# Optimization experiments

Hardware: AMD Instinct MI355X
Metric: run time of the kernel (lower is better)

Reference implementation:

```python
import jax, jax.numpy as jnp
import numpy as np

EPS = 1e-5       # BatchNorm2d eps
NHEAD = 8
FILL = -1e30     # stands in for scores_fill_value=-inf (finite for grad safety)


def _proj(x, w, b, g, beta, mean, var):
    # Conv2d 1x1 over NCHW (H=1) == channel matmul, followed by eval-mode BatchNorm2d.
    y = jnp.einsum('oc,bcht->boht', w, x) + b[None, :, None, None]
    inv = g * jax.lax.rsqrt(var + EPS)
    return y * inv[None, :, None, None] + (beta - mean * inv)[None, :, None, None]


def setup_inputs() -> dict:
    rng = jax.random.key(0)
    ks = jax.random.split(rng, 10)
    B, C, T = 8, 512, 1024
    query = jax.random.normal(ks[0], (B, C, 1, T), jnp.float32)
    key = jax.random.normal(ks[1], (B, C, 1, T), jnp.float32)
    value = jax.random.normal(ks[2], (B, C, 1, T), jnp.float32)
    mask = jax.random.randint(ks[3], (B, 1, T, T), 0, 2).astype(jnp.int32)
    Ws = jax.random.normal(ks[4], (4, C, C), jnp.float32) * (1.0 / np.sqrt(C))
    bs = jax.random.normal(ks[5], (4, C), jnp.float32) * 0.1
    gammas = jax.random.uniform(ks[6], (4, C), jnp.float32, 0.5, 1.5)
    betas = jax.random.normal(ks[7], (4, C), jnp.float32) * 0.1
    means = jax.random.normal(ks[8], (4, C), jnp.float32) * 0.1
    vars_ = jax.random.uniform(ks[9], (4, C), jnp.float32, 0.5, 1.5)
    return dict(query=query, key=key, value=value, mask=mask, Ws=Ws, bs=bs,
                gammas=gammas, betas=betas, means=means, vars_=vars_)


def reference(query, key, value, mask, Ws, bs, gammas, betas, means, vars_):
    B, C, _, T1 = query.shape
    T2 = key.shape[3]
    h = NHEAD
    d_k = C // h
    denom = 1.0 / np.sqrt(d_k)

    q = _proj(query, Ws[0], bs[0], gammas[0], betas[0], means[0], vars_[0]).reshape(B, h, d_k, T1)
    k = _proj(key,   Ws[1], bs[1], gammas[1], betas[1], means[1], vars_[1]).reshape(B, h, d_k, T2)
    v = _proj(value, Ws[2], bs[2], gammas[2], betas[2], means[2], vars_[2]).reshape(B, h, d_k, T2)

    # scores = k^T @ q -> (B, h, T2, T1); softmax over key axis (dim=2, matching torch)
    scores = jnp.einsum('bhds,bhdt->bhst', k, q) * denom
    mask0 = jnp.transpose(mask, (0, 1, 3, 2)) == 0  # (B, 1, T2, T1)
    scores = jnp.where(mask0, FILL, scores)
    attn = jax.nn.softmax(scores, axis=2)
    attn = jnp.where(mask0, 0.0, attn)

    # x = v @ attn -> (B, h, d_k, T1) -> (B, C, 1, T1)
    x = jnp.einsum('bhds,bhst->bhdt', v, attn).reshape(B, C, 1, T1)
    out = _proj(x, Ws[3], bs[3], gammas[3], betas[3], means[3], vars_[3])

    # cache=None branch: new_cache = cat(raw key, raw value) along channel dim
    new_cache = jnp.concatenate([key, value], axis=1)
    return (out, new_cache)
```

## Files before the change

kernel.cpp:

```cpp
#include <hip/hip_runtime.h>

typedef unsigned short u16;
typedef unsigned int   u32;
typedef short  bfrag   __attribute__((ext_vector_type(8)));
typedef float  accfrag __attribute__((ext_vector_type(16)));
typedef unsigned int   u32x4 __attribute__((ext_vector_type(4)));
typedef unsigned short u16x4 __attribute__((ext_vector_type(4)));
typedef float          f32x4 __attribute__((ext_vector_type(4)));

#define B_SZ 8
#define C_SZ 512
#define T_SZ 1024
#define NH   8
#define DK   64

#define QSCL 0.18033688f

__device__ __forceinline__ u16 f2bf(float f) {
  u32 u = __float_as_uint(f);
  u = u + 0x7fffu + ((u >> 16) & 1u);
  return (u16)(u >> 16);
}

__device__ __forceinline__ float fexp2(float x) {
  return __builtin_amdgcn_exp2f(x);
}

__device__ __forceinline__ u32 cvtpk(float lo, float hi) {
  u32 r;
  asm("v_cvt_pk_bf16_f32 %0, %1, %2" : "=v"(r) : "v"(lo), "v"(hi));
  return r;
}

__device__ __forceinline__ void permswap(u32 &a, u32 &b) {
  asm volatile("v_permlane32_swap_b32 %0, %1" : "+v"(a), "+v"(b));
}

__device__ __forceinline__ void gload16(const u16* g, u16* l) {
  __builtin_amdgcn_global_load_lds(
      (const __attribute__((address_space(1))) void*)g,
      (__attribute__((address_space(3))) void*)l, 16, 0, 0);
}

__global__ void prep_wb(const float* __restrict__ Ws, const float* __restrict__ bs,
                        const float* __restrict__ gam, const float* __restrict__ beta,
                        const float* __restrict__ mean, const float* __restrict__ var,
                        u16* __restrict__ Wp, float* __restrict__ bp) {
  int bx = blockIdx.x;
  if (bx < 4096) {
    int idx = bx * 256 + threadIdx.x;
    int io = idx >> 9;
    float inv = gam[io] * rsqrtf(var[io] + 1e-5f);
    Wp[idx] = f2bf(Ws[idx] * inv);
  } else {
    int idx = (bx - 4096) * 256 + threadIdx.x;
    float inv = gam[idx] * rsqrtf(var[idx] + 1e-5f);
    bp[idx] = bs[idx] * inv + beta[idx] - mean[idx] * inv;
  }
}

__global__ void transpose_cvt(const float* __restrict__ q, const float* __restrict__ k,
                              const float* __restrict__ v, u16* __restrict__ Xt,
                              float* __restrict__ cache) {
  __shared__ float tile[32][33];
  int z = blockIdx.z;
  int src = z >> 3, b = z & 7;
  const float* in = (src == 0) ? q : ((src == 1) ? k : v);
  u16* out = Xt + (size_t)src * ((size_t)B_SZ * T_SZ * C_SZ);
  int t0 = blockIdx.x * 32, c0 = blockIdx.y * 32;
  int cy  = threadIdx.x >> 3;
  int tx4 = threadIdx.x & 7;

  f32x4 v4 = *(const f32x4*)(in + (((size_t)b * C_SZ + c0 + cy) << 10) + t0 + tx4 * 4);
  if (src >= 1) {
    int cc = c0 + cy + (src == 2 ? 512 : 0);
    *(f32x4*)(cache + ((size_t)b << 20) + ((size_t)cc << 10) + t0 + tx4 * 4) = v4;
  }
  tile[cy][tx4 * 4 + 0] = v4[0];
  tile[cy][tx4 * 4 + 1] = v4[1];
  tile[cy][tx4 * 4 + 2] = v4[2];
  tile[cy][tx4 * 4 + 3] = v4[3];
  __syncthreads();
  float w0 = tile[tx4 * 4 + 0][cy];
  float w1 = tile[tx4 * 4 + 1][cy];
  float w2 = tile[tx4 * 4 + 2][cy];
  float w3 = tile[tx4 * 4 + 3][cy];
  u32 lo = cvtpk(w0, w1), hi = cvtpk(w2, w3);
  u32* orow = (u32*)(out + (((size_t)(b << 10) + t0 + cy) * C_SZ) + c0 + tx4 * 4);
  orow[0] = lo;
  orow[1] = hi;
}

__global__ void mask_bits(const int* __restrict__ mask, u32* __restrict__ mbT) {
  int gw   = (blockIdx.x * 256 + threadIdx.x) >> 6;
  int lane = threadIdx.x & 63;
  int bt   = gw >> 1;
  int half = gw & 1;
  const int* base = mask + ((size_t)bt << 10) + half * 512 + lane;
  int b = bt >> 10, t = bt & 1023;
  u32* obase = mbT + (((size_t)b * 32 + half * 16) << 10) + t;
#pragma unroll
  for (int j = 0; j < 8; ++j) {
    unsigned long long bal = __ballot(base[j * 64] != 0);
    if (lane == 0)  obase[(size_t)(2 * j + 0) << 10] = (u32)bal;
    if (lane == 32) obase[(size_t)(2 * j + 1) << 10] = (u32)(bal >> 32);
  }
}

__launch_bounds__(256, 4)
__global__ void gemm_qkv(const u16* __restrict__ Wp, const float* __restrict__ bpA,
                         const u16* __restrict__ Xt,
                         u16* __restrict__ Qf, u16* __restrict__ Kf, u16* __restrict__ Vf) {
  __shared__ __align__(16) u16 lds[2 * 128 * 64];
  int tid = threadIdx.x;
  int src = blockIdx.z >> 3;
  int b   = blockIdx.z & 7;
  int t0 = blockIdx.x * 128;
  int o0 = blockIdx.y * 128;
  int wid = tid >> 6, lane = tid & 63;
  int ln = lane & 31, hi = lane >> 5;
  int wr = wid >> 1, wc = wid & 1;

  const u16* Wsrc = Wp + (size_t)src * 262144;
  const float* bp = bpA + src * 512;
  const u16* Xin  = Xt + (size_t)src * ((size_t)B_SZ * T_SZ * C_SZ);
  u16* Yout = (src == 0) ? Qf : (src == 1 ? Kf : Vf);

  const char* Ag = (const char*)Wsrc;
  const char* Bg = (const char*)(Xin + (((size_t)b << 10) + t0) * C_SZ);
  char* ldsA = (char*)lds;
  char* ldsB = (char*)lds + 16384;

  accfrag acc[2][2];
#pragma unroll
  for (int m2 = 0; m2 < 2; ++m2)
#pragma unroll
    for (int n2 = 0; n2 < 2; ++n2)
#pragma unroll
      for (int e = 0; e < 16; ++e) acc[m2][n2][e] = 0.f;

  int lin = tid * 16;
  u32x4 ra[4], rb[4];
#pragma unroll
  for (int it = 0; it < 4; ++it) {
    int off = lin + it * 4096;
    int r = off >> 7, cb = off & 127;
    ra[it] = *(const u32x4*)(Ag + (size_t)(o0 + r) * 1024 + cb);
    rb[it] = *(const u32x4*)(Bg + (size_t)r * 1024 + cb);
  }

  for (int kt = 0; kt < 8; ++kt) {
    __syncthreads();
#pragma unroll
    for (int it = 0; it < 4; ++it) {
      int off = lin + it * 4096;
      int swz = off ^ (((off >> 7) & 7) << 4);
      *(u32x4*)(ldsA + swz) = ra[it];
      *(u32x4*)(ldsB + swz) = rb[it];
    }
    __syncthreads();
    if (kt < 7) {
#pragma unroll
      for (int it = 0; it < 4; ++it) {
        int off = lin + it * 4096;
        int r = off >> 7, cb = off & 127;
        ra[it] = *(const u32x4*)(Ag + (size_t)(o0 + r) * 1024 + (kt + 1) * 128 + cb);
        rb[it] = *(const u32x4*)(Bg + (size_t)r * 1024 + (kt + 1) * 128 + cb);
      }
    }
#pragma unroll
    for (int kk = 0; kk < 4; ++kk) {
      int csw = (kk * 32 + hi * 16) ^ ((ln & 7) << 4);
      bfrag a[2], bb[2];
#pragma unroll
      for (int m2 = 0; m2 < 2; ++m2)
        a[m2] = *(const bfrag*)(ldsA + (wr * 64 + m2 * 32 + ln) * 128 + csw);
#pragma unroll
      for (int n2 = 0; n2 < 2; ++n2)
        bb[n2] = *(const bfrag*)(ldsB + (wc * 64 + n2 * 32 + ln) * 128 + csw);
#pragma unroll
      for (int m2 = 0; m2 < 2; ++m2)
#pragma unroll
        for (int n2 = 0; n2 < 2; ++n2)
          acc[m2][n2] = __builtin_amdgcn_mfma_f32_32x32x16_bf16(a[m2], bb[n2], acc[m2][n2], 0, 0, 0);
    }
  }

  float oscl = (src == 0) ? QSCL : 1.0f;
#pragma unroll
  for (int m2 = 0; m2 < 2; ++m2) {
    int obase = o0 + wr * 64 + m2 * 32;
#pragma unroll
    for (int n2 = 0; n2 < 2; ++n2) {
      int t = t0 + wc * 64 + n2 * 32 + ln;
      if (src < 2) {
        int tt5 = t & 31, st = t >> 5;
#pragma unroll
        for (int g = 0; g < 4; ++g) {
          int d0 = obase + 8 * g + 4 * hi;
          int hh = d0 >> 6, dd = d0 & 63;
          u16x4 pk4;
#pragma unroll
          for (int qq = 0; qq < 4; ++qq)
            pk4[qq] = f2bf((acc[m2][n2][4 * g + qq] + bp[d0 + qq]) * oscl);
          size_t a = ((((size_t)b * 8 + hh) * 32 + st) << 11)
                   + (size_t)((dd >> 4) * 512 + (tt5 + 32 * ((dd >> 3) & 1)) * 8 + (dd & 7));
          *(u16x4*)(Yout + a) = pk4;
        }
      } else {
        int s = t, st = s >> 5;
#pragma unroll
        for (int r = 0; r < 16; ++r) {
          int d = obase + (r & 3) + 8 * (r >> 2) + 4 * hi;
          int hh = d >> 6, dd = d & 63;
          int fi = ((s >> 4) & 1) * 2 + ((dd >> 5) & 1);
          int l  = (dd & 31) + ((s >> 3) & 1) * 32;
          Yout[((((size_t)b * 8 + hh) * 32 + st) << 11)
               + (size_t)(fi * 512 + l * 8 + (s & 7))] = f2bf(acc[m2][n2][r] + bp[d]);
        }
      }
    }
  }
}

__launch_bounds__(256, 4)
__global__ void gemm_out(const u16* __restrict__ Wp, const float* __restrict__ bp,
                         const u16* __restrict__ Xin, float* __restrict__ Yout) {
  __shared__ __align__(16) char ldsc[24576];
  int tid = threadIdx.x;
  int b  = blockIdx.z;
  int t0 = blockIdx.x * 64;
  int o0 = blockIdx.y * 128;
  int wid = tid >> 6, lane = tid & 63;
  int ln = lane & 31, hi = lane >> 5;
  int wr = wid >> 1, wc = wid & 1;

  const char* Ag = (const char*)Wp;
  const char* Bg = (const char*)(Xin + (((size_t)b << 10) + t0) * C_SZ);
  char* ldsA = ldsc;
  char* ldsB = ldsc + 16384;

  accfrag acc[2];
#pragma unroll
  for (int m2 = 0; m2 < 2; ++m2)
#pragma unroll
    for (int e = 0; e < 16; ++e) acc[m2][e] = 0.f;

  int lin = tid * 16;
  u32x4 ra[4], rb[2];
#pragma unroll
  for (int it = 0; it < 4; ++it) {
    int off = lin + it * 4096;
    int r = off >> 7, cb = off & 127;
    ra[it] = *(const u32x4*)(Ag + (size_t)(o0 + r) * 1024 + cb);
  }
#pragma unroll
  for (int it = 0; it < 2; ++it) {
    int off = lin + it * 4096;
    int r = off >> 7, cb = off & 127;
    rb[it] = *(const u32x4*)(Bg + (size_t)r * 1024 + cb);
  }

  for (int kt = 0; kt < 8; ++kt) {
    __syncthreads();
#pragma unroll
    for (int it = 0; it < 4; ++it) {
      int off = lin + it * 4096;
      int swz = off ^ (((off >> 7) & 7) << 4);
      *(u32x4*)(ldsA + swz) = ra[it];
    }
#pragma unroll
    for (int it = 0; it < 2; ++it) {
      int off = lin + it * 4096;
      int swz = off ^ (((off >> 7) & 7) << 4);
      *(u32x4*)(ldsB + swz) = rb[it];
    }
    __syncthreads();
    if (kt < 7) {
#pragma unroll
      for (int it = 0; it < 4; ++it) {
        int off = lin + it * 4096;
        int r = off >> 7, cb = off & 127;
        ra[it] = *(const u32x4*)(Ag + (size_t)(o0 + r) * 1024 + (kt + 1) * 128 + cb);
      }
#pragma unroll
      for (int it = 0; it < 2; ++it) {
        int off = lin + it * 4096;
        int r = off >> 7, cb = off & 127;
        rb[it] = *(const u32x4*)(Bg + (size_t)r * 1024 + (kt + 1) * 128 + cb);
      }
    }
#pragma unroll
    for (int kk = 0; kk < 4; ++kk) {
      int csw = (kk * 32 + hi * 16) ^ ((ln & 7) << 4);
      bfrag a[2], bb;
#pragma unroll
      for (int m2 = 0; m2 < 2; ++m2)
        a[m2] = *(const bfrag*)(ldsA + (wr * 64 + m2 * 32 + ln) * 128 + csw);
      bb = *(const bfrag*)(ldsB + (wc * 32 + ln) * 128 + csw);
#pragma unroll
      for (int m2 = 0; m2 < 2; ++m2)
        acc[m2] = __builtin_amdgcn_mfma_f32_32x32x16_bf16(a[m2], bb, acc[m2], 0, 0, 0);
    }
  }

#pragma unroll
  for (int m2 = 0; m2 < 2; ++m2) {
    int obase = o0 + wr * 64 + m2 * 32;
    int t = t0 + wc * 32 + ln;
#pragma unroll
    for (int r = 0; r < 16; ++r) {
      int o = obase + (r & 3) + 8 * (r >> 2) + 4 * hi;
      Yout[(((size_t)b * C_SZ + o) << 10) + t] = acc[m2][r] + bp[o];
    }
  }
}

__launch_bounds__(512, 4)
__global__ void attn_fused(const u16* __restrict__ Qf, const u16* __restrict__ Kf,
                           const u16* __restrict__ Vf, const u32* __restrict__ mbT,
                           u16* __restrict__ X2) {
  __shared__ __align__(16) char smem[33 * 1024];
  u16*   sK   = (u16*)smem;
  u16*   sV   = (u16*)(smem + 16384);
  float* comb = (float*)smem;
  float* mlb  = (float*)(smem + 32768);

  int n = blockIdx.x;
  int bh = n & 63, tb = n >> 6;
  int b = bh >> 3, h = bh & 7;
  int tid = threadIdx.x;
  int wid = tid >> 6, lane = tid & 63;
  int grp = wid >> 2, wl = wid & 3;
  int ln = lane & 31, hi = lane >> 5;
  int tt = tb * 4 + wl;
  int t  = tt * 32 + ln;

  const u16* QfT = Qf + (((size_t)bh * 32 + tt) << 11);
  bfrag qf[4];
#pragma unroll
  for (int j = 0; j < 4; ++j)
    qf[j] = *(const bfrag*)(QfT + j * 512 + lane * 8);

  const u16* KfB = Kf + ((size_t)bh << 16);
  const u16* VfB = Vf + ((size_t)bh << 16);
  const u32* mcol = mbT + ((size_t)b << 15) + t;

  float m_run = -1.0e4f, l_run = 0.f;
  accfrag accd[2];
#pragma unroll
  for (int m2 = 0; m2 < 2; ++m2)
#pragma unroll
    for (int e = 0; e < 16; ++e) accd[m2][e] = 0.f;

  int gtid = tid & 255;
  int soff = gtid * 8;
  u16* sKg = sK + grp * 4096;
  u16* sVg = sV + grp * 4096;
  int st0 = grp * 16;

  gload16(KfB + ((size_t)st0 << 11) + soff, sKg + soff);
  gload16(VfB + ((size_t)st0 << 11) + soff, sVg + soff);
  u32 mw = mcol[st0 << 10];
  __syncthreads();

#pragma unroll 2
  for (int it = 0; it < 16; ++it) {
    int cur = it & 1, nxt = cur ^ 1;
    int st = st0 + it;
    u32 mn = 0;
    if (it < 15) {
      size_t tn = (size_t)(st + 1) << 11;
      gload16(KfB + tn + soff, sKg + nxt * 2048 + soff);
      gload16(VfB + tn + soff, sVg + nxt * 2048 + soff);
      mn = mcol[(st + 1) << 10];
    }

    bfrag kf[4], vf[4];
#pragma unroll
    for (int j = 0; j < 4; ++j) {
      kf[j] = *(const bfrag*)(sKg + cur * 2048 + j * 512 + lane * 8);
      vf[j] = *(const bfrag*)(sVg + cur * 2048 + j * 512 + lane * 8);
    }

    accfrag S;
#pragma unroll
    for (int e = 0; e < 16; ++e) S[e] = 0.f;
    __builtin_amdgcn_s_setprio(1);
#pragma unroll
    for (int j = 0; j < 4; ++j)
      S = __builtin_amdgcn_mfma_f32_32x32x16_bf16(kf[j], qf[j], S, 0, 0, 0);
    __builtin_amdgcn_s_setprio(0);

    u32 mbits = mw >> (4 * hi);
    float p[16];
#pragma unroll
    for (int r = 0; r < 16; ++r) {
      int pos = (r & 3) + 8 * (r >> 2);
      p[r] = ((mbits >> pos) & 1u) ? S[r] : -1e30f;
    }
    float q8[8], q4[4];
#pragma unroll
    for (int r = 0; r < 8; ++r) q8[r] = fmaxf(p[r], p[r + 8]);
#pragma unroll
    for (int r = 0; r < 4; ++r) q4[r] = fmaxf(q8[r], q8[r + 4]);
    float pmax = fmaxf(fmaxf(q4[0], q4[1]), fmaxf(q4[2], q4[3]));
    pmax = fmaxf(pmax, __shfl_xor(pmax, 32));

    if (__any(pmax > m_run + 11.5f)) {
      float m_new = fmaxf(m_run, pmax);
      float alpha = fexp2(m_run - m_new);
      l_run *= alpha;
#pragma unroll
      for (int m2 = 0; m2 < 2; ++m2)
#pragma unroll
        for (int e = 0; e < 16; ++e) accd[m2][e] *= alpha;
      m_run = m_new;
    }

#pragma unroll
    for (int r = 0; r < 16; ++r)
      p[r] = fexp2(p[r] - m_run);
    float s8[8], s4[4];
#pragma unroll
    for (int r = 0; r < 8; ++r) s8[r] = p[r] + p[r + 8];
#pragma unroll
    for (int r = 0; r < 4; ++r) s4[r] = s8[r] + s8[r + 4];
    float psum = (s4[0] + s4[1]) + (s4[2] + s4[3]);
    psum += __shfl_xor(psum, 32);
    l_run += psum;

    bfrag pf[2];
#pragma unroll
    for (int j2 = 0; j2 < 2; ++j2) {
      u32 A0 = cvtpk(p[8 * j2 + 0], p[8 * j2 + 1]);
      u32 A1 = cvtpk(p[8 * j2 + 2], p[8 * j2 + 3]);
      u32 B0 = cvtpk(p[8 * j2 + 4], p[8 * j2 + 5]);
      u32 B1 = cvtpk(p[8 * j2 + 6], p[8 * j2 + 7]);
      permswap(A0, B0);
      permswap(A1, B1);
      union { u32 u[4]; bfrag f; } pu;
      pu.u[0] = A0; pu.u[1] = A1; pu.u[2] = B0; pu.u[3] = B1;
      pf[j2] = pu.f;
    }
    __builtin_amdgcn_s_setprio(1);
#pragma unroll
    for (int j2 = 0; j2 < 2; ++j2)
#pragma unroll
      for (int m2 = 0; m2 < 2; ++m2)
        accd[m2] = __builtin_amdgcn_mfma_f32_32x32x16_bf16(vf[j2 * 2 + m2], pf[j2], accd[m2], 0, 0, 0);
    __builtin_amdgcn_s_setprio(0);

    __syncthreads();
    mw = mn;
  }

  if (grp == 1) {
#pragma unroll
    for (int m2 = 0; m2 < 2; ++m2)
#pragma unroll
      for (int e = 0; e < 16; ++e)
        comb[wl * 2048 + (m2 * 16 + e) * 64 + lane] = accd[m2][e];
    if (hi == 0) {
      mlb[(wl * 32 + ln) * 2]     = m_run;
      mlb[(wl * 32 + ln) * 2 + 1] = l_run;
    }
  }
  __syncthreads();
  if (grp == 0) {
    float m1v = mlb[(wl * 32 + ln) * 2];
    float l1v = mlb[(wl * 32 + ln) * 2 + 1];
    float M  = fmaxf(m_run, m1v);
    float w0 = fexp2(m_run - M), w1 = fexp2(m1v - M);
    float l  = l_run * w0 + l1v * w1;
    float invl = (l > 0.f) ? 1.f / l : 0.f;
    u16* Orow = X2 + (((size_t)b << 10) + t) * C_SZ + h * DK;
#pragma unroll
    for (int m2 = 0; m2 < 2; ++m2)
#pragma unroll
      for (int g = 0; g < 4; ++g) {
        u16x4 pk4;
#pragma unroll
        for (int qq = 0; qq < 4; ++qq) {
          int e = 4 * g + qq;
          float v2 = comb[wl * 2048 + (m2 * 16 + e) * 64 + lane];
          pk4[qq] = f2bf((accd[m2][e] * w0 + v2 * w1) * invl);
        }
        *(u16x4*)(Orow + m2 * 32 + 8 * g + 4 * hi) = pk4;
      }
  }
}

extern "C" void kernel_launch(void* const* d_in, const int* in_sizes, int n_in,
                              void* d_out, int out_size, void* d_ws, size_t ws_size,
                              hipStream_t stream) {
  (void)in_sizes; (void)n_in; (void)out_size; (void)ws_size;
  const float* q    = (const float*)d_in[0];
  const float* k    = (const float*)d_in[1];
  const float* v    = (const float*)d_in[2];
  const int*   mask = (const int*)d_in[3];
  const float* Ws   = (const float*)d_in[4];
  const float* bs   = (const float*)d_in[5];
  const float* gam  = (const float*)d_in[6];
  const float* beta = (const float*)d_in[7];
  const float* mean = (const float*)d_in[8];
  const float* var  = (const float*)d_in[9];

  float* out   = (float*)d_out;
  float* cache = out + (size_t)B_SZ * C_SZ * T_SZ;

  const size_t ARR = (size_t)B_SZ * T_SZ * C_SZ;
  char* ws = (char*)d_ws;
  u16*   Wp = (u16*)(ws);
  float* bp = (float*)(ws + 2097152);
  u16*   Xt = (u16*)(ws + 2162688);
  u16*   Qt = Xt + 3 * ARR;
  u16*   Kt = Qt + ARR;
  u16*   Vb = Kt + ARR;
  u16*   X2 = Vb + ARR;
  u32*   mb = (u32*)((char*)(X2 + ARR));

  prep_wb<<<4104, 256, 0, stream>>>(Ws, bs, gam, beta, mean, var, Wp, bp);
  transpose_cvt<<<dim3(32, 16, 24), 256, 0, stream>>>(q, k, v, Xt, cache);
  mask_bits<<<4096, 256, 0, stream>>>(mask, mb);

  gemm_qkv<<<dim3(8, 4, 24), 256, 0, stream>>>(Wp, bp, Xt, Qt, Kt, Vb);
  attn_fused<<<512, 512, 0, stream>>>(Qt, Kt, Vb, mb, X2);
  gemm_out<<<dim3(16, 4, 8), 256, 0, stream>>>(Wp + 786432, bp + 1536, X2, out);
}
```

Baseline: 95.30 us.

## Merge mask packing into prep kernel and double attention K/V tile per barrier

Folds the mask bit-packing kernel into the weight/bias prep kernel, removing one launch. In the attention kernel each pipeline stage now loads two 32-key tiles of K and V (with two mask words) and processes them before one barrier, halving the barrier count and making each prefetch larger. LDS use doubles to about 65 KB and launch bounds drop to 2 blocks per CU, so occupancy may fall.

```diff
diff --git a/kernel.cpp b/kernel.cpp
--- a/kernel.cpp
+++ b/kernel.cpp
@@ -42,20 +42,36 @@
       (__attribute__((address_space(3))) void*)l, 16, 0, 0);
 }
 
-__global__ void prep_wb(const float* __restrict__ Ws, const float* __restrict__ bs,
-                        const float* __restrict__ gam, const float* __restrict__ beta,
-                        const float* __restrict__ mean, const float* __restrict__ var,
-                        u16* __restrict__ Wp, float* __restrict__ bp) {
+__global__ void prep_mask(const float* __restrict__ Ws, const float* __restrict__ bs,
+                          const float* __restrict__ gam, const float* __restrict__ beta,
+                          const float* __restrict__ mean, const float* __restrict__ var,
+                          const int* __restrict__ mask,
+                          u16* __restrict__ Wp, float* __restrict__ bp,
+                          u32* __restrict__ mbT) {
   int bx = blockIdx.x;
   if (bx < 4096) {
     int idx = bx * 256 + threadIdx.x;
     int io = idx >> 9;
     float inv = gam[io] * rsqrtf(var[io] + 1e-5f);
     Wp[idx] = f2bf(Ws[idx] * inv);
-  } else {
+  } else if (bx < 4104) {
     int idx = (bx - 4096) * 256 + threadIdx.x;
     float inv = gam[idx] * rsqrtf(var[idx] + 1e-5f);
     bp[idx] = bs[idx] * inv + beta[idx] - mean[idx] * inv;
+  } else {
+    int gw   = ((bx - 4104) * 256 + threadIdx.x) >> 6;
+    int lane = threadIdx.x & 63;
+    int bt   = gw >> 1;
+    int half = gw & 1;
+    const int* base = mask + ((size_t)bt << 10) + half * 512 + lane;
+    int b = bt >> 10, t = bt & 1023;
+    u32* obase = mbT + (((size_t)b * 32 + half * 16) << 10) + t;
+#pragma unroll
+    for (int j = 0; j < 8; ++j) {
+      unsigned long long bal = __ballot(base[j * 64] != 0);
+      if (lane == 0)  obase[(size_t)(2 * j + 0) << 10] = (u32)bal;
+      if (lane == 32) obase[(size_t)(2 * j + 1) << 10] = (u32)(bal >> 32);
+    }
   }
 }
 
@@ -91,22 +107,6 @@
   orow[1] = hi;
 }
 
-__global__ void mask_bits(const int* __restrict__ mask, u32* __restrict__ mbT) {
-  int gw   = (blockIdx.x * 256 + threadIdx.x) >> 6;
-  int lane = threadIdx.x & 63;
-  int bt   = gw >> 1;
-  int half = gw & 1;
-  const int* base = mask + ((size_t)bt << 10) + half * 512 + lane;
-  int b = bt >> 10, t = bt & 1023;
-  u32* obase = mbT + (((size_t)b * 32 + half * 16) << 10) + t;
-#pragma unroll
-  for (int j = 0; j < 8; ++j) {
-    unsigned long long bal = __ballot(base[j * 64] != 0);
-    if (lane == 0)  obase[(size_t)(2 * j + 0) << 10] = (u32)bal;
-    if (lane == 32) obase[(size_t)(2 * j + 1) << 10] = (u32)(bal >> 32);
-  }
-}
-
 __launch_bounds__(256, 4)
 __global__ void gemm_qkv(const u16* __restrict__ Wp, const float* __restrict__ bpA,
                          const u16* __restrict__ Xt,
@@ -316,15 +316,15 @@
   }
 }
 
-__launch_bounds__(512, 4)
+__launch_bounds__(512, 2)
 __global__ void attn_fused(const u16* __restrict__ Qf, const u16* __restrict__ Kf,
                            const u16* __restrict__ Vf, const u32* __restrict__ mbT,
                            u16* __restrict__ X2) {
-  __shared__ __align__(16) char smem[33 * 1024];
-  u16*   sK   = (u16*)smem;
-  u16*   sV   = (u16*)(smem + 16384);
+  __shared__ __align__(16) char smem[66560];
+  u16*   sKa  = (u16*)smem;
+  u16*   sVa  = (u16*)(smem + 32768);
   float* comb = (float*)smem;
-  float* mlb  = (float*)(smem + 32768);
+  float* mlb  = (float*)(smem + 65536);
 
   int n = blockIdx.x;
   int bh = n & 63, tb = n >> 6;
@@ -355,104 +355,117 @@
 
   int gtid = tid & 255;
   int soff = gtid * 8;
-  u16* sKg = sK + grp * 4096;
-  u16* sVg = sV + grp * 4096;
-  int st0 = grp * 16;
-
-  gload16(KfB + ((size_t)st0 << 11) + soff, sKg + soff);
-  gload16(VfB + ((size_t)st0 << 11) + soff, sVg + soff);
-  u32 mw = mcol[st0 << 10];
+  u16* sKg = sKa + grp * 8192;
+  u16* sVg = sVa + grp * 8192;
+  int sp0 = grp * 8;
+
+  {
+    size_t pb = (size_t)(sp0 * 2) << 11;
+    gload16(KfB + pb + soff,        sKg + soff);
+    gload16(KfB + pb + 2048 + soff, sKg + 2048 + soff);
+    gload16(VfB + pb + soff,        sVg + soff);
+    gload16(VfB + pb + 2048 + soff, sVg + 2048 + soff);
+  }
+  u32 mw0 = mcol[(size_t)(sp0 * 2) << 10];
+  u32 mw1 = mcol[(size_t)(sp0 * 2 + 1) << 10];
   __syncthreads();
 
 #pragma unroll 2
-  for (int it = 0; it < 16; ++it) {
+  for (int it = 0; it < 8; ++it) {
     int cur = it & 1, nxt = cur ^ 1;
-    int st = st0 + it;
-    u32 mn = 0;
-    if (it < 15) {
-      size_t tn = (size_t)(st + 1) << 11;
-      gload16(KfB + tn + soff, sKg + nxt * 2048 + soff);
-      gload16(VfB + tn + soff, sVg + nxt * 2048 + soff);
-      mn = mcol[(st + 1) << 10];
-    }
-
-    bfrag kf[4], vf[4];
-#pragma unroll
-    for (int j = 0; j < 4; ++j) {
-      kf[j] = *(const bfrag*)(sKg + cur * 2048 + j * 512 + lane * 8);
-      vf[j] = *(const bfrag*)(sVg + cur * 2048 + j * 512 + lane * 8);
-    }
-
-    accfrag S;
-#pragma unroll
-    for (int e = 0; e < 16; ++e) S[e] = 0.f;
-    __builtin_amdgcn_s_setprio(1);
-#pragma unroll
-    for (int j = 0; j < 4; ++j)
-      S = __builtin_amdgcn_mfma_f32_32x32x16_bf16(kf[j], qf[j], S, 0, 0, 0);
-    __builtin_amdgcn_s_setprio(0);
-
-    u32 mbits = mw >> (4 * hi);
-    float p[16];
-#pragma unroll
-    for (int r = 0; r < 16; ++r) {
-      int pos = (r & 3) + 8 * (r >> 2);
-      p[r] = ((mbits >> pos) & 1u) ? S[r] : -1e30f;
-    }
-    float q8[8], q4[4];
-#pragma unroll
-    for (int r = 0; r < 8; ++r) q8[r] = fmaxf(p[r], p[r + 8]);
-#pragma unroll
-    for (int r = 0; r < 4; ++r) q4[r] = fmaxf(q8[r], q8[r + 4]);
-    float pmax = fmaxf(fmaxf(q4[0], q4[1]), fmaxf(q4[2], q4[3]));
-    pmax = fmaxf(pmax, __shfl_xor(pmax, 32));
-
-    if (__any(pmax > m_run + 11.5f)) {
-      float m_new = fmaxf(m_run, pmax);
-      float alpha = fexp2(m_run - m_new);
-      l_run *= alpha;
-#pragma unroll
-      for (int m2 = 0; m2 < 2; ++m2)
-#pragma unroll
-        for (int e = 0; e < 16; ++e) accd[m2][e] *= alpha;
-      m_run = m_new;
-    }
-
-#pragma unroll
-    for (int r = 0; r < 16; ++r)
-      p[r] = fexp2(p[r] - m_run);
-    float s8[8], s4[4];
-#pragma unroll
-    for (int r = 0; r < 8; ++r) s8[r] = p[r] + p[r + 8];
-#pragma unroll
-    for (int r = 0; r < 4; ++r) s4[r] = s8[r] + s8[r + 4];
-    float psum = (s4[0] + s4[1]) + (s4[2] + s4[3]);
-    psum += __shfl_xor(psum, 32);
-    l_run += psum;
-
-    bfrag pf[2];
-#pragma unroll
-    for (int j2 = 0; j2 < 2; ++j2) {
-      u32 A0 = cvtpk(p[8 * j2 + 0], p[8 * j2 + 1]);
-      u32 A1 = cvtpk(p[8 * j2 + 2], p[8 * j2 + 3]);
-      u32 B0 = cvtpk(p[8 * j2 + 4], p[8 * j2 + 5]);
-      u32 B1 = cvtpk(p[8 * j2 + 6], p[8 * j2 + 7]);
-      permswap(A0, B0);
-      permswap(A1, B1);
-      union { u32 u[4]; bfrag f; } pu;
-      pu.u[0] = A0; pu.u[1] = A1; pu.u[2] = B0; pu.u[3] = B1;
-      pf[j2] = pu.f;
-    }
-    __builtin_amdgcn_s_setprio(1);
-#pragma unroll
-    for (int j2 = 0; j2 < 2; ++j2)
-#pragma unroll
-      for (int m2 = 0; m2 < 2; ++m2)
-        accd[m2] = __builtin_amdgcn_mfma_f32_32x32x16_bf16(vf[j2 * 2 + m2], pf[j2], accd[m2], 0, 0, 0);
-    __builtin_amdgcn_s_setprio(0);
+    u32 mn0 = 0, mn1 = 0;
+    if (it < 7) {
+      size_t pb = (size_t)((sp0 + it + 1) * 2) << 11;
+      gload16(KfB + pb + soff,        sKg + nxt * 4096 + soff);
+      gload16(KfB + pb + 2048 + soff, sKg + nxt * 4096 + 2048 + soff);
+      gload16(VfB + pb + soff,        sVg + nxt * 4096 + soff);
+      gload16(VfB + pb + 2048 + soff, sVg + nxt * 4096 + 2048 + soff);
+      mn0 = mcol[(size_t)((sp0 + it + 1) * 2) << 10];
+      mn1 = mcol[(size_t)((sp0 + it + 1) * 2 + 1) << 10];
+    }
+
+#pragma unroll
+    for (int sub = 0; sub < 2; ++sub) {
+      u32 mw = (sub == 0) ? mw0 : mw1;
+      bfrag kf[4], vf[4];
+#pragma unroll
+      for (int j = 0; j < 4; ++j) {
+        kf[j] = *(const bfrag*)(sKg + cur * 4096 + sub * 2048 + j * 512 + lane * 8);
+        vf[j] = *(const bfrag*)(sVg + cur * 4096 + sub * 2048 + j * 512 + lane * 8);
+      }
+
+      accfrag S;
+#pragma unroll
+      for (int e = 0; e < 16; ++e) S[e] = 0.f;
+      __builtin_amdgcn_s_setprio(1);
+#pragma unroll
+      for (int j = 0; j < 4; ++j)
+        S = __builtin_amdgcn_mfma_f32_32x32x16_bf16(kf[j], qf[j], S, 0, 0, 0);
+      __builtin_amdgcn_s_setprio(0);
+
+      u32 mbits = mw >> (4 * hi);
+      float p[16];
+#pragma unroll
+      for (int r = 0; r < 16; ++r) {
+        int pos = (r & 3) + 8 * (r >> 2);
+        p[r] = ((mbits >> pos) & 1u) ? S[r] : -1e30f;
+      }
+      float q8[8], q4[4];
+#pragma unroll
+      for (int r = 0; r < 8; ++r) q8[r] = fmaxf(p[r], p[r + 8]);
+#pragma unroll
+      for (int r = 0; r < 4; ++r) q4[r] = fmaxf(q8[r], q8[r + 4]);
+      float pmax = fmaxf(fmaxf(q4[0], q4[1]), fmaxf(q4[2], q4[3]));
+      pmax = fmaxf(pmax, __shfl_xor(pmax, 32));
+
+      if (__any(pmax > m_run + 11.5f)) {
+        float m_new = fmaxf(m_run, pmax);
+        float alpha = fexp2(m_run - m_new);
+        l_run *= alpha;
+#pragma unroll
+        for (int m2 = 0; m2 < 2; ++m2)
+#pragma unroll
+          for (int e = 0; e < 16; ++e) accd[m2][e] *= alpha;
+        m_run = m_new;
+      }
+
+#pragma unroll
+      for (int r = 0; r < 16; ++r)
+        p[r] = fexp2(p[r] - m_run);
+      float s8[8], s4[4];
+#pragma unroll
+      for (int r = 0; r < 8; ++r) s8[r] = p[r] + p[r + 8];
+#pragma unroll
+      for (int r = 0; r < 4; ++r) s4[r] = s8[r] + s8[r + 4];
+      float psum = (s4[0] + s4[1]) + (s4[2] + s4[3]);
+      psum += __shfl_xor(psum, 32);
+      l_run += psum;
+
+      bfrag pf[2];
+#pragma unroll
+      for (int j2 = 0; j2 < 2; ++j2) {
+        u32 A0 = cvtpk(p[8 * j2 + 0], p[8 * j2 + 1]);
+        u32 A1 = cvtpk(p[8 * j2 + 2], p[8 * j2 + 3]);
+        u32 B0 = cvtpk(p[8 * j2 + 4], p[8 * j2 + 5]);
+        u32 B1 = cvtpk(p[8 * j2 + 6], p[8 * j2 + 7]);
+        permswap(A0, B0);
+        permswap(A1, B1);
+        union { u32 u[4]; bfrag f; } pu;
+        pu.u[0] = A0; pu.u[1] = A1; pu.u[2] = B0; pu.u[3] = B1;
+        pf[j2] = pu.f;
+      }
+      __builtin_amdgcn_s_setprio(1);
+#pragma unroll
+      for (int j2 = 0; j2 < 2; ++j2)
+#pragma unroll
+        for (int m2 = 0; m2 < 2; ++m2)
+          accd[m2] = __builtin_amdgcn_mfma_f32_32x32x16_bf16(vf[j2 * 2 + m2], pf[j2], accd[m2], 0, 0, 0);
+      __builtin_amdgcn_s_setprio(0);
+    }
 
     __syncthreads();
-    mw = mn;
+    mw0 = mn0;
+    mw1 = mn1;
   }
 
   if (grp == 1) {
@@ -520,9 +533,8 @@
   u16*   X2 = Vb + ARR;
   u32*   mb = (u32*)((char*)(X2 + ARR));
 
-  prep_wb<<<4104, 256, 0, stream>>>(Ws, bs, gam, beta, mean, var, Wp, bp);
+  prep_mask<<<8200, 256, 0, stream>>>(Ws, bs, gam, beta, mean, var, mask, Wp, bp, mb);
   transpose_cvt<<<dim3(32, 16, 24), 256, 0, stream>>>(q, k, v, Xt, cache);
-  mask_bits<<<4096, 256, 0, stream>>>(mask, mb);
 
   gemm_qkv<<<dim3(8, 4, 24), 256, 0, stream>>>(Wp, bp, Xt, Qt, Kt, Vb);
   attn_fused<<<512, 512, 0, stream>>>(Qt, Kt, Vb, mb, X2);
```

Measured after the change: 93.49 us. About the same (-1.9%).
